# Kernel optimization log

Measured on AMD Instinct MI355X. Metric: run time of the kernel, lower is better.

The kernel has to match this reference:

```python
import jax, jax.numpy as jnp
import numpy as np


def setup_inputs() -> dict:
    key = jax.random.key(0)
    k1, k2 = jax.random.split(key)
    x = jax.random.normal(k1, (8, 8192, 128), dtype=jnp.float32)
    embed = jax.random.normal(k2, (1024, 128), dtype=jnp.float32)
    return {"x": x, "embed": embed}


def reference(x, embed):
    """EuclideanCodebook.forward, eval mode, c=0 (Euclidean path).

    x:     [..., D] inputs
    embed: [K, D] codebook
    Returns (quantize [..., D], embed_ind [...]).
    """
    shape = x.shape
    xf = x.reshape(-1, shape[-1])                      # (N, D)
    x2 = jnp.sum(xf * xf, axis=1, keepdims=True)       # (N, 1)
    e2 = jnp.sum(embed * embed, axis=1)                # (K,)
    dist = -(x2 - 2.0 * (xf @ embed.T) + e2[None, :])  # (N, K)
    embed_ind = jnp.argmax(dist, axis=-1)              # (N,)
    embed_ind = embed_ind.reshape(shape[:-1])          # postprocess_emb
    quantize = embed[embed_ind]                        # dequantize (gather)
    return quantize, embed_ind
```

## Files before the change

### kernel.cpp

```cpp
#include <hip/hip_runtime.h>

typedef _Float16 half8 __attribute__((ext_vector_type(8)));
typedef float f32x4 __attribute__((ext_vector_type(4)));
typedef unsigned int u32x4 __attribute__((ext_vector_type(4)));

#define DD 128


__global__ void prep_kernel(const float* __restrict__ embed,
                            char* __restrict__ frag,
                            float* __restrict__ e2neg, int total) {
  int t = blockIdx.x * blockDim.x + threadIdx.x;
  if (t >= total) return;
  int lane = t & 63;
  int idx = (t >> 6) & 7;
  int c = t >> 9;
  int s = idx >> 1;
  int hl = idx & 1;
  int n = c * 16 + (lane & 15);
  int kb = s * 32 + ((lane >> 4) << 3);
  const float* src = embed + (size_t)n * DD + kb;
  _Float16* dst = (_Float16*)(frag + (size_t)c * 8192 + idx * 1024 + lane * 16);
#pragma unroll
  for (int j = 0; j < 8; ++j) {
    float v = src[j];
    _Float16 hi = (_Float16)v;
    dst[j] = hl ? (_Float16)(v - (float)hi) : hi;
  }
  if (idx == 0) {
    const float* e = embed + (size_t)n * DD;
    double acc = 0.0;
    for (int j = 0; j < DD; ++j) { double v = (double)e[j]; acc += v * v; }
    e2neg[c * 64 + lane] = (float)(-acc);
  }
}

__global__ __launch_bounds__(256) void vq_argmin_kernel(
    const float* __restrict__ x, const float* __restrict__ embed,
    const char* __restrict__ wsf, const float* __restrict__ wse,
    float* __restrict__ out_q, float* __restrict__ out_i, int nch) {
  const int lane = threadIdx.x & 63;
  const int w = threadIdx.x >> 6;
  const int m16 = lane & 15;
  const int g = lane >> 4;
  const int row0 = blockIdx.x * 128 + w * 32;

  __shared__ alignas(16) char lds[2][8192];

  half8 ah[2][4], al[2][4];
#pragma unroll
  for (int t = 0; t < 2; ++t) {
    const float* xrow = x + (size_t)(row0 + t * 16 + m16) * DD;
#pragma unroll
    for (int s = 0; s < 4; ++s) {
      const float* p = xrow + s * 32 + g * 8;
      f32x4 v0 = *(const f32x4*)(p);
      f32x4 v1 = *(const f32x4*)(p + 4);
#pragma unroll
      for (int j = 0; j < 4; ++j) {
        float v = v0[j];
        _Float16 hi = (_Float16)v;
        ah[t][s][j] = hi;
        al[t][s][j] = (_Float16)(v - (float)hi);
      }
#pragma unroll
      for (int j = 0; j < 4; ++j) {
        float v = v1[j];
        _Float16 hi = (_Float16)v;
        ah[t][s][4 + j] = hi;
        al[t][s][4 + j] = (_Float16)(v - (float)hi);
      }
    }
  }

  float bestv0[4], bestv1[4];
  int besti0[4], besti1[4];
#pragma unroll
  for (int r = 0; r < 4; ++r) {
    bestv0[r] = -__builtin_inff();
    bestv1[r] = -__builtin_inff();
    besti0[r] = 0;
    besti1[r] = 0;
  }

  {
    const char* gs = wsf + (size_t)0 * 8192 + w * 2048 + lane * 16;
    u32x4 s0 = *(const u32x4*)(gs);
    u32x4 s1 = *(const u32x4*)(gs + 1024);
    char* lw = &lds[0][w * 2048 + lane * 16];
    *(u32x4*)(lw) = s0;
    *(u32x4*)(lw + 1024) = s1;
  }
  __syncthreads();

  for (int c = 0; c < nch; ++c) {
    const int buf = c & 1;
    u32x4 t0, t1;
    const bool pre = (c + 1 < nch);
    if (pre) {
      const char* gs = wsf + (size_t)(c + 1) * 8192 + w * 2048 + lane * 16;
      t0 = *(const u32x4*)(gs);
      t1 = *(const u32x4*)(gs + 1024);
    }
    const float ne_ = wse[(size_t)c * 64 + lane];

    const char* fb = &lds[buf][0];
    half8 bh[4], bl[4];
#pragma unroll
    for (int s = 0; s < 4; ++s) {
      bh[s] = *(const half8*)(fb + (2 * s) * 1024 + lane * 16);
      bl[s] = *(const half8*)(fb + (2 * s + 1) * 1024 + lane * 16);
    }

    f32x4 acc0 = {0.f, 0.f, 0.f, 0.f};
    f32x4 acc1 = {0.f, 0.f, 0.f, 0.f};
#pragma unroll
    for (int s = 0; s < 4; ++s) {
      acc0 = __builtin_amdgcn_mfma_f32_16x16x32_f16(ah[0][s], bh[s], acc0, 0,
                                                    0, 0);
      acc1 = __builtin_amdgcn_mfma_f32_16x16x32_f16(ah[1][s], bh[s], acc1, 0,
                                                    0, 0);
      acc0 = __builtin_amdgcn_mfma_f32_16x16x32_f16(al[0][s], bh[s], acc0, 0,
                                                    0, 0);
      acc1 = __builtin_amdgcn_mfma_f32_16x16x32_f16(al[1][s], bh[s], acc1, 0,
                                                    0, 0);
      acc0 = __builtin_amdgcn_mfma_f32_16x16x32_f16(ah[0][s], bl[s], acc0, 0,
                                                    0, 0);
      acc1 = __builtin_amdgcn_mfma_f32_16x16x32_f16(ah[1][s], bl[s], acc1, 0,
                                                    0, 0);
    }
    const int n_ = c * 16 + m16;
#pragma unroll
    for (int r = 0; r < 4; ++r) {
      float s0 = fmaf(2.f, acc0[r], ne_);
      if (s0 > bestv0[r]) { bestv0[r] = s0; besti0[r] = n_; }
      float s1 = fmaf(2.f, acc1[r], ne_);
      if (s1 > bestv1[r]) { bestv1[r] = s1; besti1[r] = n_; }
    }

    if (pre) {
      char* lw = &lds[buf ^ 1][w * 2048 + lane * 16];
      *(u32x4*)(lw) = t0;
      *(u32x4*)(lw + 1024) = t1;
    }
    __syncthreads();
  }

#pragma unroll
  for (int off = 1; off < 16; off <<= 1) {
#pragma unroll
    for (int r = 0; r < 4; ++r) {
      float ov0 = __shfl_xor(bestv0[r], off, 64);
      int oi0 = __shfl_xor(besti0[r], off, 64);
      if (ov0 > bestv0[r] || (ov0 == bestv0[r] && oi0 < besti0[r])) {
        bestv0[r] = ov0;
        besti0[r] = oi0;
      }
      float ov1 = __shfl_xor(bestv1[r], off, 64);
      int oi1 = __shfl_xor(besti1[r], off, 64);
      if (ov1 > bestv1[r] || (ov1 == bestv1[r] && oi1 < besti1[r])) {
        bestv1[r] = ov1;
        besti1[r] = oi1;
      }
    }
  }

#pragma unroll
  for (int t = 0; t < 2; ++t) {
#pragma unroll
    for (int r = 0; r < 4; ++r) {
      const int row = row0 + t * 16 + g * 4 + r;
      const int idx = t ? besti1[r] : besti0[r];
      if (m16 == 0) out_i[row] = (float)idx;
      const f32x4* src = (const f32x4*)(embed + (size_t)idx * DD) + m16 * 2;
      f32x4* dst = (f32x4*)(out_q + (size_t)row * DD) + m16 * 2;
      dst[0] = src[0];
      dst[1] = src[1];
    }
  }
}

__global__ void vq_fallback_kernel(const float* __restrict__ x,
                                   const float* __restrict__ embed,
                                   float* __restrict__ out_q,
                                   float* __restrict__ out_i, int N, int K) {
  int row = blockIdx.x * blockDim.x + threadIdx.x;
  if (row >= N) return;
  const float* xr = x + (size_t)row * DD;
  float xv[DD];
  for (int j = 0; j < DD; ++j) xv[j] = xr[j];
  double best = -1e300;
  int bi = 0;
  for (int k = 0; k < K; ++k) {
    const float* e = embed + (size_t)k * DD;
    double acc = 0.0;
    for (int j = 0; j < DD; ++j) {
      double d = (double)xv[j] - (double)e[j];
      acc += d * d;
    }
    double sc = -acc;
    if (sc > best) { best = sc; bi = k; }
  }
  out_i[row] = (float)bi;
  for (int j = 0; j < DD; ++j)
    out_q[(size_t)row * DD + j] = embed[(size_t)bi * DD + j];
}

extern "C" void kernel_launch(void* const* d_in, const int* in_sizes, int n_in,
                              void* d_out, int out_size, void* d_ws,
                              size_t ws_size, hipStream_t stream) {
  const float* x = (const float*)d_in[0];
  const float* embed = (const float*)d_in[1];
  const int N = in_sizes[0] / DD;
  const int K = in_sizes[1] / DD;
  float* out_q = (float*)d_out;
  float* out_i = out_q + (size_t)N * DD;

  const int nch = K / 16;
  const size_t frag_bytes = (size_t)nch * 8192;
  const size_t e2_bytes = (size_t)nch * 256;
  const size_t need = frag_bytes + e2_bytes;

  if (ws_size < need || (N % 128) != 0 || (K % 16) != 0) {
    vq_fallback_kernel<<<(N + 255) / 256, 256, 0, stream>>>(x, embed, out_q,
                                                            out_i, N, K);
    return;
  }

  char* wsf = (char*)d_ws;
  float* wse = (float*)(wsf + frag_bytes);

  const int total_f = nch * 8 * 64;
  prep_kernel<<<(total_f + 255) / 256, 256, 0, stream>>>(embed, wsf, wse,
                                                         total_f);
  vq_argmin_kernel<<<N / 128, 256, 0, stream>>>(x, embed, wsf, wse, out_q,
                                                out_i, nch);
}
```

Measured before the change: 65.20 us.

## Split codebook across wave pairs per block and merge argmax via LDS

```diff
diff --git a/kernel.cpp b/kernel.cpp
--- a/kernel.cpp
+++ b/kernel.cpp
@@ -35,19 +35,9 @@
   }
 }
 
-__global__ __launch_bounds__(256) void vq_argmin_kernel(
-    const float* __restrict__ x, const float* __restrict__ embed,
-    const char* __restrict__ wsf, const float* __restrict__ wse,
-    float* __restrict__ out_q, float* __restrict__ out_i, int nch) {
-  const int lane = threadIdx.x & 63;
-  const int w = threadIdx.x >> 6;
-  const int m16 = lane & 15;
-  const int g = lane >> 4;
-  const int row0 = blockIdx.x * 128 + w * 32;
-
-  __shared__ alignas(16) char lds[2][8192];
-
-  half8 ah[2][4], al[2][4];
+__device__ __forceinline__ void load_a_frags(const float* __restrict__ x,
+                                             int row0, int m16, int g,
+                                             half8 ah[2][4], half8 al[2][4]) {
 #pragma unroll
   for (int t = 0; t < 2; ++t) {
     const float* xrow = x + (size_t)(row0 + t * 16 + m16) * DD;
@@ -72,6 +62,30 @@
       }
     }
   }
+}
+
+__global__ __launch_bounds__(256, 3) void vq_argmin_kernel(
+    const float* __restrict__ x, const float* __restrict__ embed,
+    const char* __restrict__ wsf, const float* __restrict__ wse,
+    float* __restrict__ out_q, float* __restrict__ out_i, int nch) {
+  const int tid = threadIdx.x;
+  const int lane = tid & 63;
+  const int w = tid >> 6;
+  const int m16 = lane & 15;
+  const int g = lane >> 4;
+  const int row0 = blockIdx.x * 64 + (w & 1) * 32;
+  const int kh = w >> 1;
+  const int nsteps = nch >> 1;
+  const int pairLane = ((w & 1) << 6) | lane;
+
+  __shared__ alignas(16) char lds_frag[2][2][8192];
+  __shared__ float lds_e2[1024];
+
+  for (int i = tid; i < nch * 16; i += 256)
+    lds_e2[i] = wse[(size_t)(i >> 4) * 64 + (i & 15)];
+
+  half8 ah[2][4], al[2][4];
+  load_a_frags(x, row0, m16, g, ah, al);
 
   float bestv0[4], bestv1[4];
   int besti0[4], besti1[4];
@@ -84,52 +98,61 @@
   }
 
   {
-    const char* gs = wsf + (size_t)0 * 8192 + w * 2048 + lane * 16;
+    const char* gs = wsf + (size_t)(kh * nsteps) * 8192 + pairLane * 16;
     u32x4 s0 = *(const u32x4*)(gs);
-    u32x4 s1 = *(const u32x4*)(gs + 1024);
-    char* lw = &lds[0][w * 2048 + lane * 16];
+    u32x4 s1 = *(const u32x4*)(gs + 2048);
+    u32x4 s2 = *(const u32x4*)(gs + 4096);
+    u32x4 s3 = *(const u32x4*)(gs + 6144);
+    char* lw = &lds_frag[0][kh][pairLane * 16];
     *(u32x4*)(lw) = s0;
-    *(u32x4*)(lw + 1024) = s1;
+    *(u32x4*)(lw + 2048) = s1;
+    *(u32x4*)(lw + 4096) = s2;
+    *(u32x4*)(lw + 6144) = s3;
   }
   __syncthreads();
 
-  for (int c = 0; c < nch; ++c) {
-    const int buf = c & 1;
-    u32x4 t0, t1;
-    const bool pre = (c + 1 < nch);
+  for (int s = 0; s < nsteps; ++s) {
+    const int buf = s & 1;
+    u32x4 t0, t1, t2, t3;
+    const bool pre = (s + 1 < nsteps);
     if (pre) {
-      const char* gs = wsf + (size_t)(c + 1) * 8192 + w * 2048 + lane * 16;
+      const char* gs =
+          wsf + (size_t)(kh * nsteps + s + 1) * 8192 + pairLane * 16;
       t0 = *(const u32x4*)(gs);
-      t1 = *(const u32x4*)(gs + 1024);
-    }
-    const float ne_ = wse[(size_t)c * 64 + lane];
-
-    const char* fb = &lds[buf][0];
+      t1 = *(const u32x4*)(gs + 2048);
+      t2 = *(const u32x4*)(gs + 4096);
+      t3 = *(const u32x4*)(gs + 6144);
+    }
+
+    const int chnk = kh * nsteps + s;
+    const float ne_ = lds_e2[chnk * 16 + m16];
+
+    const char* fb = &lds_frag[buf][kh][0];
     half8 bh[4], bl[4];
 #pragma unroll
-    for (int s = 0; s < 4; ++s) {
-      bh[s] = *(const half8*)(fb + (2 * s) * 1024 + lane * 16);
-      bl[s] = *(const half8*)(fb + (2 * s + 1) * 1024 + lane * 16);
+    for (int q = 0; q < 4; ++q) {
+      bh[q] = *(const half8*)(fb + (2 * q) * 1024 + lane * 16);
+      bl[q] = *(const half8*)(fb + (2 * q + 1) * 1024 + lane * 16);
     }
 
     f32x4 acc0 = {0.f, 0.f, 0.f, 0.f};
     f32x4 acc1 = {0.f, 0.f, 0.f, 0.f};
 #pragma unroll
-    for (int s = 0; s < 4; ++s) {
-      acc0 = __builtin_amdgcn_mfma_f32_16x16x32_f16(ah[0][s], bh[s], acc0, 0,
-                                                    0, 0);
-      acc1 = __builtin_amdgcn_mfma_f32_16x16x32_f16(ah[1][s], bh[s], acc1, 0,
-                                                    0, 0);
-      acc0 = __builtin_amdgcn_mfma_f32_16x16x32_f16(al[0][s], bh[s], acc0, 0,
-                                                    0, 0);
-      acc1 = __builtin_amdgcn_mfma_f32_16x16x32_f16(al[1][s], bh[s], acc1, 0,
-                                                    0, 0);
-      acc0 = __builtin_amdgcn_mfma_f32_16x16x32_f16(ah[0][s], bl[s], acc0, 0,
-                                                    0, 0);
-      acc1 = __builtin_amdgcn_mfma_f32_16x16x32_f16(ah[1][s], bl[s], acc1, 0,
-                                                    0, 0);
-    }
-    const int n_ = c * 16 + m16;
+    for (int q = 0; q < 4; ++q) {
+      acc0 = __builtin_amdgcn_mfma_f32_16x16x32_f16(ah[0][q], bh[q], acc0, 0,
+                                                    0, 0);
+      acc1 = __builtin_amdgcn_mfma_f32_16x16x32_f16(ah[1][q], bh[q], acc1, 0,
+                                                    0, 0);
+      acc0 = __builtin_amdgcn_mfma_f32_16x16x32_f16(al[0][q], bh[q], acc0, 0,
+                                                    0, 0);
+      acc1 = __builtin_amdgcn_mfma_f32_16x16x32_f16(al[1][q], bh[q], acc1, 0,
+                                                    0, 0);
+      acc0 = __builtin_amdgcn_mfma_f32_16x16x32_f16(ah[0][q], bl[q], acc0, 0,
+                                                    0, 0);
+      acc1 = __builtin_amdgcn_mfma_f32_16x16x32_f16(ah[1][q], bl[q], acc1, 0,
+                                                    0, 0);
+    }
+    const int n_ = chnk * 16 + m16;
 #pragma unroll
     for (int r = 0; r < 4; ++r) {
       float s0 = fmaf(2.f, acc0[r], ne_);
@@ -139,11 +162,49 @@
     }
 
     if (pre) {
-      char* lw = &lds[buf ^ 1][w * 2048 + lane * 16];
+      char* lw = &lds_frag[buf ^ 1][kh][pairLane * 16];
       *(u32x4*)(lw) = t0;
-      *(u32x4*)(lw + 1024) = t1;
+      *(u32x4*)(lw + 2048) = t1;
+      *(u32x4*)(lw + 4096) = t2;
+      *(u32x4*)(lw + 6144) = t3;
     }
     __syncthreads();
+  }
+
+  float* vbuf = (float*)&lds_frag[0][0][0];
+  int* ibuf = (int*)&lds_frag[0][1][0];
+  if (w >= 2) {
+    float* vb = vbuf + ((w - 2) * 64 + lane) * 8;
+    int* ib = ibuf + ((w - 2) * 64 + lane) * 8;
+#pragma unroll
+    for (int r = 0; r < 4; ++r) {
+      vb[r] = bestv0[r];
+      vb[4 + r] = bestv1[r];
+      ib[r] = besti0[r];
+      ib[4 + r] = besti1[r];
+    }
+  }
+  __syncthreads();
+  if (w >= 2) return;
+
+  {
+    const float* vb = vbuf + (w * 64 + lane) * 8;
+    const int* ib = ibuf + (w * 64 + lane) * 8;
+#pragma unroll
+    for (int r = 0; r < 4; ++r) {
+      float pv0 = vb[r];
+      int pi0 = ib[r];
+      if (pv0 > bestv0[r] || (pv0 == bestv0[r] && pi0 < besti0[r])) {
+        bestv0[r] = pv0;
+        besti0[r] = pi0;
+      }
+      float pv1 = vb[4 + r];
+      int pi1 = ib[4 + r];
+      if (pv1 > bestv1[r] || (pv1 == bestv1[r] && pi1 < besti1[r])) {
+        bestv1[r] = pv1;
+        besti1[r] = pi1;
+      }
+    }
   }
 
 #pragma unroll
@@ -221,7 +282,8 @@
   const size_t e2_bytes = (size_t)nch * 256;
   const size_t need = frag_bytes + e2_bytes;
 
-  if (ws_size < need || (N % 128) != 0 || (K % 16) != 0) {
+  if (ws_size < need || (N % 64) != 0 || (K % 16) != 0 || (nch % 2) != 0 ||
+      nch > 64) {
     vq_fallback_kernel<<<(N + 255) / 256, 256, 0, stream>>>(x, embed, out_q,
                                                             out_i, N, K);
     return;
@@ -233,6 +295,6 @@
   const int total_f = nch * 8 * 64;
   prep_kernel<<<(total_f + 255) / 256, 256, 0, stream>>>(embed, wsf, wse,
                                                          total_f);
-  vq_argmin_kernel<<<N / 128, 256, 0, stream>>>(x, embed, wsf, wse, out_q,
-                                                out_i, nch);
-}
+  vq_argmin_kernel<<<N / 64, 256, 0, stream>>>(x, embed, wsf, wse, out_q,
+                                               out_i, nch);
+}
```

Result: slower. 68.55 us (+5.1%).

## Split codebook across four blocks per row tile and merge partial argmins

Applied to the files above, without the earlier changes.

```diff
diff --git a/kernel.cpp b/kernel.cpp
--- a/kernel.cpp
+++ b/kernel.cpp
@@ -35,17 +35,20 @@
   }
 }
 
-__global__ __launch_bounds__(256) void vq_argmin_kernel(
-    const float* __restrict__ x, const float* __restrict__ embed,
-    const char* __restrict__ wsf, const float* __restrict__ wse,
-    float* __restrict__ out_q, float* __restrict__ out_i, int nch) {
-  const int lane = threadIdx.x & 63;
-  const int w = threadIdx.x >> 6;
+__global__ __launch_bounds__(256, 4) void vq_pass1(
+    const float* __restrict__ x, const char* __restrict__ wsf,
+    const float* __restrict__ wse, float* __restrict__ wsv,
+    int* __restrict__ wsi, int N) {
+  const int tid = threadIdx.x;
+  const int lane = tid & 63;
+  const int w = tid >> 6;
   const int m16 = lane & 15;
   const int g = lane >> 4;
-  const int row0 = blockIdx.x * 128 + w * 32;
-
-  __shared__ alignas(16) char lds[2][8192];
+  const int rowblk = blockIdx.x >> 2;
+  const int slice = blockIdx.x & 3;
+  const int row0 = rowblk * 128 + w * 32;
+
+  __shared__ alignas(16) char lds_b[32768];
 
   half8 ah[2][4], al[2][4];
 #pragma unroll
@@ -83,65 +86,54 @@
     besti1[r] = 0;
   }
 
-  {
-    const char* gs = wsf + (size_t)0 * 8192 + w * 2048 + lane * 16;
-    u32x4 s0 = *(const u32x4*)(gs);
-    u32x4 s1 = *(const u32x4*)(gs + 1024);
-    char* lw = &lds[0][w * 2048 + lane * 16];
-    *(u32x4*)(lw) = s0;
-    *(u32x4*)(lw + 1024) = s1;
-  }
-  __syncthreads();
-
-  for (int c = 0; c < nch; ++c) {
-    const int buf = c & 1;
-    u32x4 t0, t1;
-    const bool pre = (c + 1 < nch);
-    if (pre) {
-      const char* gs = wsf + (size_t)(c + 1) * 8192 + w * 2048 + lane * 16;
-      t0 = *(const u32x4*)(gs);
-      t1 = *(const u32x4*)(gs + 1024);
-    }
-    const float ne_ = wse[(size_t)c * 64 + lane];
-
-    const char* fb = &lds[buf][0];
-    half8 bh[4], bl[4];
-#pragma unroll
-    for (int s = 0; s < 4; ++s) {
-      bh[s] = *(const half8*)(fb + (2 * s) * 1024 + lane * 16);
-      bl[s] = *(const half8*)(fb + (2 * s + 1) * 1024 + lane * 16);
-    }
-
-    f32x4 acc0 = {0.f, 0.f, 0.f, 0.f};
-    f32x4 acc1 = {0.f, 0.f, 0.f, 0.f};
-#pragma unroll
-    for (int s = 0; s < 4; ++s) {
-      acc0 = __builtin_amdgcn_mfma_f32_16x16x32_f16(ah[0][s], bh[s], acc0, 0,
-                                                    0, 0);
-      acc1 = __builtin_amdgcn_mfma_f32_16x16x32_f16(ah[1][s], bh[s], acc1, 0,
-                                                    0, 0);
-      acc0 = __builtin_amdgcn_mfma_f32_16x16x32_f16(al[0][s], bh[s], acc0, 0,
-                                                    0, 0);
-      acc1 = __builtin_amdgcn_mfma_f32_16x16x32_f16(al[1][s], bh[s], acc1, 0,
-                                                    0, 0);
-      acc0 = __builtin_amdgcn_mfma_f32_16x16x32_f16(ah[0][s], bl[s], acc0, 0,
-                                                    0, 0);
-      acc1 = __builtin_amdgcn_mfma_f32_16x16x32_f16(ah[1][s], bl[s], acc1, 0,
-                                                    0, 0);
-    }
-    const int n_ = c * 16 + m16;
-#pragma unroll
-    for (int r = 0; r < 4; ++r) {
-      float s0 = fmaf(2.f, acc0[r], ne_);
-      if (s0 > bestv0[r]) { bestv0[r] = s0; besti0[r] = n_; }
-      float s1 = fmaf(2.f, acc1[r], ne_);
-      if (s1 > bestv1[r]) { bestv1[r] = s1; besti1[r] = n_; }
-    }
-
-    if (pre) {
-      char* lw = &lds[buf ^ 1][w * 2048 + lane * 16];
-      *(u32x4*)(lw) = t0;
-      *(u32x4*)(lw + 1024) = t1;
+  for (int u = 0; u < 4; ++u) {
+    {
+      const char* gs = wsf + ((size_t)slice * 16 + u * 4) * 8192;
+#pragma unroll
+      for (int i = 0; i < 8; ++i) {
+        const int off = (tid + i * 256) * 16;
+        *(u32x4*)(lds_b + off) = *(const u32x4*)(gs + off);
+      }
+    }
+    __syncthreads();
+
+#pragma unroll
+    for (int cc = 0; cc < 4; ++cc) {
+      const int cg = slice * 16 + u * 4 + cc;
+      const char* fb = lds_b + cc * 8192;
+      half8 bh[4], bl[4];
+#pragma unroll
+      for (int s = 0; s < 4; ++s) {
+        bh[s] = *(const half8*)(fb + (2 * s) * 1024 + lane * 16);
+        bl[s] = *(const half8*)(fb + (2 * s + 1) * 1024 + lane * 16);
+      }
+      const float ne_ = wse[(size_t)cg * 64 + lane];
+
+      f32x4 acc0 = {0.f, 0.f, 0.f, 0.f};
+      f32x4 acc1 = {0.f, 0.f, 0.f, 0.f};
+#pragma unroll
+      for (int s = 0; s < 4; ++s) {
+        acc0 = __builtin_amdgcn_mfma_f32_16x16x32_f16(ah[0][s], bh[s], acc0, 0,
+                                                      0, 0);
+        acc1 = __builtin_amdgcn_mfma_f32_16x16x32_f16(ah[1][s], bh[s], acc1, 0,
+                                                      0, 0);
+        acc0 = __builtin_amdgcn_mfma_f32_16x16x32_f16(al[0][s], bh[s], acc0, 0,
+                                                      0, 0);
+        acc1 = __builtin_amdgcn_mfma_f32_16x16x32_f16(al[1][s], bh[s], acc1, 0,
+                                                      0, 0);
+        acc0 = __builtin_amdgcn_mfma_f32_16x16x32_f16(ah[0][s], bl[s], acc0, 0,
+                                                      0, 0);
+        acc1 = __builtin_amdgcn_mfma_f32_16x16x32_f16(ah[1][s], bl[s], acc1, 0,
+                                                      0, 0);
+      }
+      const int n_ = cg * 16 + m16;
+#pragma unroll
+      for (int r = 0; r < 4; ++r) {
+        float s0 = fmaf(2.f, acc0[r], ne_);
+        if (s0 > bestv0[r]) { bestv0[r] = s0; besti0[r] = n_; }
+        float s1 = fmaf(2.f, acc1[r], ne_);
+        if (s1 > bestv1[r]) { bestv1[r] = s1; besti1[r] = n_; }
+      }
     }
     __syncthreads();
   }
@@ -165,18 +157,50 @@
     }
   }
 
-#pragma unroll
-  for (int t = 0; t < 2; ++t) {
-#pragma unroll
-    for (int r = 0; r < 4; ++r) {
-      const int row = row0 + t * 16 + g * 4 + r;
-      const int idx = t ? besti1[r] : besti0[r];
-      if (m16 == 0) out_i[row] = (float)idx;
-      const f32x4* src = (const f32x4*)(embed + (size_t)idx * DD) + m16 * 2;
-      f32x4* dst = (f32x4*)(out_q + (size_t)row * DD) + m16 * 2;
-      dst[0] = src[0];
-      dst[1] = src[1];
-    }
+  if (m16 == 0) {
+#pragma unroll
+    for (int t = 0; t < 2; ++t) {
+#pragma unroll
+      for (int r = 0; r < 4; ++r) {
+        const int row = row0 + t * 16 + g * 4 + r;
+        wsv[(size_t)slice * N + row] = t ? bestv1[r] : bestv0[r];
+        wsi[(size_t)slice * N + row] = t ? besti1[r] : besti0[r];
+      }
+    }
+  }
+}
+
+__global__ __launch_bounds__(256) void vq_merge(
+    const float* __restrict__ embed, const float* __restrict__ wsv,
+    const int* __restrict__ wsi, float* __restrict__ out_q,
+    float* __restrict__ out_i, int N) {
+  const int tid = threadIdx.x;
+  const int r = blockIdx.x * 256 + tid;
+  __shared__ int idxs[256];
+
+  float bv = -__builtin_inff();
+  int bi = 0;
+#pragma unroll
+  for (int s = 0; s < 4; ++s) {
+    float v = wsv[(size_t)s * N + r];
+    int i = wsi[(size_t)s * N + r];
+    if (v > bv || (v == bv && i < bi)) { bv = v; bi = i; }
+  }
+  out_i[r] = (float)bi;
+  idxs[tid] = bi;
+  __syncthreads();
+
+  const int w = tid >> 6;
+  const int lane = tid & 63;
+  const int l32 = lane & 31;
+  const int hl = lane >> 5;
+  const size_t rbase = (size_t)blockIdx.x * 256;
+#pragma unroll 4
+  for (int it = 0; it < 32; ++it) {
+    const int lr = w * 64 + it * 2 + hl;
+    const int idx = idxs[lr];
+    f32x4 v = *((const f32x4*)(embed + (size_t)idx * DD) + l32);
+    *((f32x4*)(out_q + (rbase + lr) * DD) + l32) = v;
   }
 }
 
@@ -219,9 +243,10 @@
   const int nch = K / 16;
   const size_t frag_bytes = (size_t)nch * 8192;
   const size_t e2_bytes = (size_t)nch * 256;
-  const size_t need = frag_bytes + e2_bytes;
-
-  if (ws_size < need || (N % 128) != 0 || (K % 16) != 0) {
+  const size_t vi_bytes = (size_t)4 * N * 4;
+  const size_t need = frag_bytes + e2_bytes + 2 * vi_bytes;
+
+  if (ws_size < need || (N % 256) != 0 || (K % 256) != 0) {
     vq_fallback_kernel<<<(N + 255) / 256, 256, 0, stream>>>(x, embed, out_q,
                                                             out_i, N, K);
     return;
@@ -229,10 +254,12 @@
 
   char* wsf = (char*)d_ws;
   float* wse = (float*)(wsf + frag_bytes);
+  float* wsv = (float*)(wsf + frag_bytes + e2_bytes);
+  int* wsi = (int*)(wsf + frag_bytes + e2_bytes + vi_bytes);
 
   const int total_f = nch * 8 * 64;
   prep_kernel<<<(total_f + 255) / 256, 256, 0, stream>>>(embed, wsf, wse,
                                                          total_f);
-  vq_argmin_kernel<<<N / 128, 256, 0, stream>>>(x, embed, wsf, wse, out_q,
-                                                out_i, nch);
-}
+  vq_pass1<<<(N / 128) * 4, 256, 0, stream>>>(x, wsf, wse, wsv, wsi, N);
+  vq_merge<<<N / 256, 256, 0, stream>>>(embed, wsv, wsi, out_q, out_i, N);
+}
```

New measurement: 80.46 us. 23.4% more time.
